# Kernel tuning notes

Measured on AMD Instinct MI355X. Metric: run time of the kernel, lower is better.

The kernel has to match this reference:

```python
import jax, jax.numpy as jnp
import numpy as np
from jax import lax


def setup_inputs() -> dict:
    key = jax.random.key(0)
    k1, k2, k3 = jax.random.split(key, 3)
    B, F, L = 16384, 1024, 3
    x = jax.random.normal(k1, (B, F), dtype=jnp.float32)
    # xavier_uniform on [F,1]: bound = sqrt(6/(F+1))
    bound = float(np.sqrt(6.0 / (F + 1)))
    kernels = jax.random.uniform(k2, (L, F, 1), dtype=jnp.float32, minval=-bound, maxval=bound)
    bias = jax.random.uniform(k3, (L, F, 1), dtype=jnp.float32, minval=-bound, maxval=bound)
    return {"x": x, "kernels": kernels, "bias": bias}


def reference(x, kernels, bias):
    # DCN vector cross: xl_{i+1} = x0 * (xl . w_i) + b_i + xl
    x0 = x  # [B, F]

    def step(xl, wb):
        w, b = wb  # w: [F,1], b: [F,1]
        s = xl @ w[:, 0]                     # [B]  (xl^T w per batch row)
        xl_new = x0 * s[:, None] + b[:, 0] + xl  # [B, F]
        return xl_new, None

    xl, _ = lax.scan(step, x0, (kernels, bias))
    return xl
```

## Files before the change

kernel.cpp:

```cpp
#include <hip/hip_runtime.h>


constexpr int B = 16384;
constexpr int F = 1024;
constexpr int L = 3;
constexpr int ROWS_PER_BLOCK = 4;
constexpr int BLOCK = 64 * ROWS_PER_BLOCK;

__global__ __launch_bounds__(BLOCK) void cross_layer_kernel(
    const float* __restrict__ x,
    const float* __restrict__ kernels,
    const float* __restrict__ bias,
    float* __restrict__ out)
{
    const int lane = threadIdx.x & 63;
    const int wave = threadIdx.x >> 6;
    const int row  = blockIdx.x * ROWS_PER_BLOCK + wave;
    if (row >= B) return;

    const float4* xrow = (const float4*)(x + (size_t)row * F);

    float4 x0[4], xl[4];
#pragma unroll
    for (int c = 0; c < 4; ++c) {
        x0[c] = xrow[c * 64 + lane];
        xl[c] = x0[c];
    }

#pragma unroll
    for (int l = 0; l < L; ++l) {
        const float4* wv = (const float4*)(kernels + (size_t)l * F);
        const float4* bv = (const float4*)(bias    + (size_t)l * F);
        float4 w[4], b[4];
#pragma unroll
        for (int c = 0; c < 4; ++c) {
            w[c] = wv[c * 64 + lane];
            b[c] = bv[c * 64 + lane];
        }

        float s = 0.0f;
#pragma unroll
        for (int c = 0; c < 4; ++c) {
            s = fmaf(xl[c].x, w[c].x, s);
            s = fmaf(xl[c].y, w[c].y, s);
            s = fmaf(xl[c].z, w[c].z, s);
            s = fmaf(xl[c].w, w[c].w, s);
        }

#pragma unroll
        for (int off = 32; off >= 1; off >>= 1)
            s += __shfl_xor(s, off, 64);

#pragma unroll
        for (int c = 0; c < 4; ++c) {
            xl[c].x = fmaf(x0[c].x, s, b[c].x + xl[c].x);
            xl[c].y = fmaf(x0[c].y, s, b[c].y + xl[c].y);
            xl[c].z = fmaf(x0[c].z, s, b[c].z + xl[c].z);
            xl[c].w = fmaf(x0[c].w, s, b[c].w + xl[c].w);
        }
    }

    float4* orow = (float4*)(out + (size_t)row * F);
#pragma unroll
    for (int c = 0; c < 4; ++c)
        orow[c * 64 + lane] = xl[c];
}

extern "C" void kernel_launch(void* const* d_in, const int* in_sizes, int n_in,
                              void* d_out, int out_size, void* d_ws, size_t ws_size,
                              hipStream_t stream) {
    const float* x       = (const float*)d_in[0];
    const float* kernels = (const float*)d_in[1];
    const float* bias    = (const float*)d_in[2];
    float* out           = (float*)d_out;

    dim3 grid(B / ROWS_PER_BLOCK);
    dim3 block(BLOCK);
    cross_layer_kernel<<<grid, block, 0, stream>>>(x, kernels, bias, out);
}
```

Measured before the change: 123.0 us.

## Collapse three cross layers into closed-form scalar recurrence with fused dot products

Rewrites the three sequential cross layers algebraically. Each output row is x0*S plus the summed biases, where S comes from six dot products (x0·w_i and b_j·w_k) computed in one pass and reduced with a single interleaved shuffle tree. This removes the serial dependence between layers, so three sequential wave reductions become one batched reduction. It adds redundant per-row bias·weight dot products and reloads of the bias vectors, and it changes the order of floating-point summation.

New measurement: 121.6 us, median of 2. No clear change (-1.2%).

```diff
diff --git a/kernel.cpp b/kernel.cpp
--- a/kernel.cpp
+++ b/kernel.cpp
@@ -3,7 +3,6 @@
 
 constexpr int B = 16384;
 constexpr int F = 1024;
-constexpr int L = 3;
 constexpr int ROWS_PER_BLOCK = 4;
 constexpr int BLOCK = 64 * ROWS_PER_BLOCK;
 
@@ -16,54 +15,78 @@
     const int lane = threadIdx.x & 63;
     const int wave = threadIdx.x >> 6;
     const int row  = blockIdx.x * ROWS_PER_BLOCK + wave;
-    if (row >= B) return;
 
     const float4* xrow = (const float4*)(x + (size_t)row * F);
+    const float4* w0v  = (const float4*)(kernels);
+    const float4* w1v  = (const float4*)(kernels + F);
+    const float4* w2v  = (const float4*)(kernels + 2 * F);
+    const float4* b0v  = (const float4*)(bias);
+    const float4* b1v  = (const float4*)(bias + F);
+    const float4* b2v  = (const float4*)(bias + 2 * F);
 
-    float4 x0[4], xl[4];
+    float4 x0[4];
+#pragma unroll
+    for (int c = 0; c < 4; ++c) x0[c] = xrow[c * 64 + lane];
+
+    float p0 = 0.f, p1 = 0.f, p2 = 0.f, p3 = 0.f, p4 = 0.f, p5 = 0.f;
 #pragma unroll
     for (int c = 0; c < 4; ++c) {
-        x0[c] = xrow[c * 64 + lane];
-        xl[c] = x0[c];
+        const int i = c * 64 + lane;
+        const float4 w0 = w0v[i];
+        const float4 w1 = w1v[i];
+        const float4 w2 = w2v[i];
+        const float4 b0 = b0v[i];
+        const float4 b1 = b1v[i];
+
+        p0 = fmaf(x0[c].x, w0.x, p0); p0 = fmaf(x0[c].y, w0.y, p0);
+        p0 = fmaf(x0[c].z, w0.z, p0); p0 = fmaf(x0[c].w, w0.w, p0);
+
+        p1 = fmaf(x0[c].x, w1.x, p1); p1 = fmaf(x0[c].y, w1.y, p1);
+        p1 = fmaf(x0[c].z, w1.z, p1); p1 = fmaf(x0[c].w, w1.w, p1);
+
+        p2 = fmaf(x0[c].x, w2.x, p2); p2 = fmaf(x0[c].y, w2.y, p2);
+        p2 = fmaf(x0[c].z, w2.z, p2); p2 = fmaf(x0[c].w, w2.w, p2);
+
+        p3 = fmaf(b0.x, w1.x, p3); p3 = fmaf(b0.y, w1.y, p3);
+        p3 = fmaf(b0.z, w1.z, p3); p3 = fmaf(b0.w, w1.w, p3);
+
+        p4 = fmaf(b0.x, w2.x, p4); p4 = fmaf(b0.y, w2.y, p4);
+        p4 = fmaf(b0.z, w2.z, p4); p4 = fmaf(b0.w, w2.w, p4);
+
+        p5 = fmaf(b1.x, w2.x, p5); p5 = fmaf(b1.y, w2.y, p5);
+        p5 = fmaf(b1.z, w2.z, p5); p5 = fmaf(b1.w, w2.w, p5);
     }
 
 #pragma unroll
-    for (int l = 0; l < L; ++l) {
-        const float4* wv = (const float4*)(kernels + (size_t)l * F);
-        const float4* bv = (const float4*)(bias    + (size_t)l * F);
-        float4 w[4], b[4];
-#pragma unroll
-        for (int c = 0; c < 4; ++c) {
-            w[c] = wv[c * 64 + lane];
-            b[c] = bv[c * 64 + lane];
-        }
+    for (int off = 32; off >= 1; off >>= 1) {
+        p0 += __shfl_xor(p0, off, 64);
+        p1 += __shfl_xor(p1, off, 64);
+        p2 += __shfl_xor(p2, off, 64);
+        p3 += __shfl_xor(p3, off, 64);
+        p4 += __shfl_xor(p4, off, 64);
+        p5 += __shfl_xor(p5, off, 64);
+    }
 
-        float s = 0.0f;
-#pragma unroll
-        for (int c = 0; c < 4; ++c) {
-            s = fmaf(xl[c].x, w[c].x, s);
-            s = fmaf(xl[c].y, w[c].y, s);
-            s = fmaf(xl[c].z, w[c].z, s);
-            s = fmaf(xl[c].w, w[c].w, s);
-        }
-
-#pragma unroll
-        for (int off = 32; off >= 1; off >>= 1)
-            s += __shfl_xor(s, off, 64);
-
-#pragma unroll
-        for (int c = 0; c < 4; ++c) {
-            xl[c].x = fmaf(x0[c].x, s, b[c].x + xl[c].x);
-            xl[c].y = fmaf(x0[c].y, s, b[c].y + xl[c].y);
-            xl[c].z = fmaf(x0[c].z, s, b[c].z + xl[c].z);
-            xl[c].w = fmaf(x0[c].w, s, b[c].w + xl[c].w);
-        }
-    }
+    const float a1 = 1.f + p0;
+    const float s1 = fmaf(a1, p1, p3);
+    const float a2 = a1 + s1;
+    const float s2 = fmaf(a2, p2, p4 + p5);
+    const float S  = a2 + s2;
 
     float4* orow = (float4*)(out + (size_t)row * F);
 #pragma unroll
-    for (int c = 0; c < 4; ++c)
-        orow[c * 64 + lane] = xl[c];
+    for (int c = 0; c < 4; ++c) {
+        const int i = c * 64 + lane;
+        const float4 b0 = b0v[i];
+        const float4 b1 = b1v[i];
+        const float4 b2 = b2v[i];
+        float4 o;
+        o.x = fmaf(x0[c].x, S, b0.x + b1.x + b2.x);
+        o.y = fmaf(x0[c].y, S, b0.y + b1.y + b2.y);
+        o.z = fmaf(x0[c].z, S, b0.z + b1.z + b2.z);
+        o.w = fmaf(x0[c].w, S, b0.w + b1.w + b2.w);
+        orow[i] = o;
+    }
 }
 
 extern "C" void kernel_launch(void* const* d_in, const int* in_sizes, int n_in,
```

## Collapse three cross layers into closed form with two rows per wave

Applied to the files above, without the earlier changes.

Rewrites the three-layer recurrence algebraically: each output row is x0 scaled by a per-row scalar plus the summed biases. The scalar comes from three dot products of x0 with the weights and three bias-weight dot products. All reductions are done in a single batched shuffle pass instead of three dependent ones. Each wave now handles two rows to amortise the weight and bias loads, and nontemporal loads and stores are used for the streamed x and output. The kernel is memory-bound, so gains depend mostly on load/store efficiency; the reassociated float math may differ slightly from the reference, and the hardcoded three-layer formula drops the generic L loop.

Result: no change. 125.0 us (+1.6%).

```diff
diff --git a/kernel.cpp b/kernel.cpp
--- a/kernel.cpp
+++ b/kernel.cpp
@@ -3,9 +3,12 @@
 
 constexpr int B = 16384;
 constexpr int F = 1024;
-constexpr int L = 3;
-constexpr int ROWS_PER_BLOCK = 4;
-constexpr int BLOCK = 64 * ROWS_PER_BLOCK;
+constexpr int ROWS_PER_WAVE = 2;
+constexpr int WAVES_PER_BLOCK = 4;
+constexpr int BLOCK = 64 * WAVES_PER_BLOCK;
+constexpr int ROWS_PER_BLOCK = ROWS_PER_WAVE * WAVES_PER_BLOCK;
+
+typedef float v4f __attribute__((ext_vector_type(4)));
 
 __global__ __launch_bounds__(BLOCK) void cross_layer_kernel(
     const float* __restrict__ x,
@@ -15,55 +18,97 @@
 {
     const int lane = threadIdx.x & 63;
     const int wave = threadIdx.x >> 6;
-    const int row  = blockIdx.x * ROWS_PER_BLOCK + wave;
-    if (row >= B) return;
+    const int row0 = (blockIdx.x * WAVES_PER_BLOCK + wave) * ROWS_PER_WAVE;
 
-    const float4* xrow = (const float4*)(x + (size_t)row * F);
+    const v4f* xa = (const v4f*)(x + (size_t)row0 * F);
+    const v4f* xb = (const v4f*)(x + (size_t)(row0 + 1) * F);
+    const v4f* w0v = (const v4f*)(kernels);
+    const v4f* w1v = (const v4f*)(kernels + F);
+    const v4f* w2v = (const v4f*)(kernels + 2 * F);
+    const v4f* b0v = (const v4f*)(bias);
+    const v4f* b1v = (const v4f*)(bias + F);
+    const v4f* b2v = (const v4f*)(bias + 2 * F);
 
-    float4 x0[4], xl[4];
+    v4f xA[4], xB[4];
 #pragma unroll
     for (int c = 0; c < 4; ++c) {
-        x0[c] = xrow[c * 64 + lane];
-        xl[c] = x0[c];
+        xA[c] = __builtin_nontemporal_load(&xa[c * 64 + lane]);
+        xB[c] = __builtin_nontemporal_load(&xb[c * 64 + lane]);
+    }
+
+    float dA0 = 0.f, dA1 = 0.f, dA2 = 0.f;
+    float dB0 = 0.f, dB1 = 0.f, dB2 = 0.f;
+    float t01 = 0.f, t02 = 0.f, t12 = 0.f;
+
+#pragma unroll
+    for (int c = 0; c < 4; ++c) {
+        const int i = c * 64 + lane;
+        const v4f w0 = w0v[i];
+        const v4f w1 = w1v[i];
+        const v4f w2 = w2v[i];
+        const v4f b0 = b0v[i];
+        const v4f b1 = b1v[i];
+
+#pragma unroll
+        for (int e = 0; e < 4; ++e) {
+            dA0 = fmaf(xA[c][e], w0[e], dA0);
+            dA1 = fmaf(xA[c][e], w1[e], dA1);
+            dA2 = fmaf(xA[c][e], w2[e], dA2);
+            dB0 = fmaf(xB[c][e], w0[e], dB0);
+            dB1 = fmaf(xB[c][e], w1[e], dB1);
+            dB2 = fmaf(xB[c][e], w2[e], dB2);
+            t01 = fmaf(b0[e], w1[e], t01);
+            t02 = fmaf(b0[e], w2[e], t02);
+            t12 = fmaf(b1[e], w2[e], t12);
+        }
     }
 
 #pragma unroll
-    for (int l = 0; l < L; ++l) {
-        const float4* wv = (const float4*)(kernels + (size_t)l * F);
-        const float4* bv = (const float4*)(bias    + (size_t)l * F);
-        float4 w[4], b[4];
-#pragma unroll
-        for (int c = 0; c < 4; ++c) {
-            w[c] = wv[c * 64 + lane];
-            b[c] = bv[c * 64 + lane];
-        }
-
-        float s = 0.0f;
-#pragma unroll
-        for (int c = 0; c < 4; ++c) {
-            s = fmaf(xl[c].x, w[c].x, s);
-            s = fmaf(xl[c].y, w[c].y, s);
-            s = fmaf(xl[c].z, w[c].z, s);
-            s = fmaf(xl[c].w, w[c].w, s);
-        }
-
-#pragma unroll
-        for (int off = 32; off >= 1; off >>= 1)
-            s += __shfl_xor(s, off, 64);
-
-#pragma unroll
-        for (int c = 0; c < 4; ++c) {
-            xl[c].x = fmaf(x0[c].x, s, b[c].x + xl[c].x);
-            xl[c].y = fmaf(x0[c].y, s, b[c].y + xl[c].y);
-            xl[c].z = fmaf(x0[c].z, s, b[c].z + xl[c].z);
-            xl[c].w = fmaf(x0[c].w, s, b[c].w + xl[c].w);
-        }
+    for (int off = 32; off >= 1; off >>= 1) {
+        dA0 += __shfl_xor(dA0, off, 64);
+        dA1 += __shfl_xor(dA1, off, 64);
+        dA2 += __shfl_xor(dA2, off, 64);
+        dB0 += __shfl_xor(dB0, off, 64);
+        dB1 += __shfl_xor(dB1, off, 64);
+        dB2 += __shfl_xor(dB2, off, 64);
+        t01 += __shfl_xor(t01, off, 64);
+        t02 += __shfl_xor(t02, off, 64);
+        t12 += __shfl_xor(t12, off, 64);
     }
 
-    float4* orow = (float4*)(out + (size_t)row * F);
+    const float tc = t02 + t12;
+    const float a1A = 1.f + dA0;
+    const float s1A = fmaf(a1A, dA1, t01);
+    const float a2A = a1A + s1A;
+    const float s2A = fmaf(a2A, dA2, tc);
+    const float SA  = a2A + s2A;
+
+    const float a1B = 1.f + dB0;
+    const float s1B = fmaf(a1B, dB1, t01);
+    const float a2B = a1B + s1B;
+    const float s2B = fmaf(a2B, dB2, tc);
+    const float SB  = a2B + s2B;
+
+    v4f* oa = (v4f*)(out + (size_t)row0 * F);
+    v4f* ob = (v4f*)(out + (size_t)(row0 + 1) * F);
 #pragma unroll
-    for (int c = 0; c < 4; ++c)
-        orow[c * 64 + lane] = xl[c];
+    for (int c = 0; c < 4; ++c) {
+        const int i = c * 64 + lane;
+        const v4f b0 = b0v[i];
+        const v4f b1 = b1v[i];
+        const v4f b2 = b2v[i];
+        v4f bs;
+#pragma unroll
+        for (int e = 0; e < 4; ++e) bs[e] = b0[e] + b1[e] + b2[e];
+        v4f oA, oB;
+#pragma unroll
+        for (int e = 0; e < 4; ++e) {
+            oA[e] = fmaf(xA[c][e], SA, bs[e]);
+            oB[e] = fmaf(xB[c][e], SB, bs[e]);
+        }
+        __builtin_nontemporal_store(oA, &oa[i]);
+        __builtin_nontemporal_store(oB, &ob[i]);
+    }
 }
 
 extern "C" void kernel_launch(void* const* d_in, const int* in_sizes, int n_in,
```
